# Performance work log

Measured on AMD Instinct MI355X. Metric: run time of the kernel, lower is better.

## Reference

```python
import jax, jax.numpy as jnp
import numpy as np
from jax import lax

B, T, C, H, N = 8, 2048, 1024, 16, 64  # dim=C=H*N


def setup_inputs() -> dict:
    key = jax.random.key(0)
    ks = jax.random.split(key, 12)
    s = 0.02
    return {
        "x": jax.random.normal(ks[0], (B, T, C), jnp.float32),
        "v_first": jnp.zeros((B, T, C), jnp.float32),  # unused for layer_id=0
        "ln1_w": jnp.ones((C,), jnp.float32),
        "ln1_b": jnp.zeros((C,), jnp.float32),
        "ln2_w": jnp.ones((C,), jnp.float32),
        "ln2_b": jnp.zeros((C,), jnp.float32),
        "w_r": jax.random.normal(ks[1], (C, C), jnp.float32) * s,
        "w_k": jax.random.normal(ks[2], (C, C), jnp.float32) * s,
        "w_v": jax.random.normal(ks[3], (C, C), jnp.float32) * s,
        "w_o": jax.random.normal(ks[4], (C, C), jnp.float32) * s,
        "w_g": jax.random.normal(ks[5], (H, C), jnp.float32) * s,
        "ck_w": jax.random.normal(ks[6], (4 * C, C), jnp.float32) * s,
        "cv_w": jax.random.normal(ks[7], (C, 4 * C), jnp.float32) * s,
    }


def _time_shift(x):
    # ZeroPad2d((0,0,1,-1)): zero at t=0, drop last timestep
    return jnp.pad(x, ((0, 0), (1, 0), (0, 0)))[:, :-1]


def _layernorm(x, w, b, eps=1e-5):
    mu = jnp.mean(x, axis=-1, keepdims=True)
    var = jnp.var(x, axis=-1, keepdims=True)
    return (x - mu) * lax.rsqrt(var + eps) * w + b


def _wkv(r, k, v):
    # wkv[0] = v[0]; wkv[t] = (wkv[t-1] + v[t]) / 2  (k is unused, faithful to source)
    vt = jnp.moveaxis(v, 1, 0)  # [T,B,H,N]

    def step(carry, v_t):
        s = 0.5 * (carry + v_t)
        return s, s

    # init carry = v[0] => first output = 0.5*(v0+v0) = v0, matching wkv[0]=v[0]
    _, out = lax.scan(step, vt[0], vt)
    return r * jnp.moveaxis(out, 0, 1)


def reference(x, v_first, ln1_w, ln1_b, ln2_w, ln2_b,
              w_r, w_k, w_v, w_o, w_g, ck_w, cv_w):
    # ---- TimeMixBiDirectional on ln1(x) ----
    h = _layernorm(x, ln1_w, ln1_b)
    xx = _time_shift(h) - h
    hs = h + xx  # == time-shifted h
    r = (hs @ w_r.T).reshape(B, T, H, N)
    k = (hs @ w_k.T).reshape(B, T, H, N)
    v_flat = hs @ w_v.T
    v_first_out = v_flat  # layer_id == 0
    v = v_flat.reshape(B, T, H, N)

    x_fwd = _wkv(r, k, v)
    x_bwd = jnp.flip(
        _wkv(jnp.flip(r, 1), jnp.flip(k, 1), jnp.flip(v, 1)), 1)

    gate = jax.nn.sigmoid(xx @ w_g.T)[..., None]  # [B,T,H,1]
    x_comb = gate * x_fwd + (1.0 - gate) * x_bwd
    attn_out = x_comb.reshape(B, T, C) @ w_o.T

    x1 = x + attn_out

    # ---- ChannelMix on ln2(x1) ----
    h2 = _layernorm(x1, ln2_w, ln2_b)
    k2 = _time_shift(h2)  # h2 + (shift(h2) - h2)
    k2 = jnp.square(jax.nn.relu(k2 @ ck_w.T))
    ffn_out = k2 @ cv_w.T

    return (x1 + ffn_out, v_first_out)
```

## Files before the change

### kernel.cpp

```cpp
#include <hip/hip_runtime.h>

constexpr int B_ = 8, T_ = 2048, C_ = 1024, H_ = 16, N_ = 64;
constexpr int M_ = B_ * T_;
constexpr int FC_ = 4 * C_;

typedef __attribute__((ext_vector_type(8))) short bf16x8;
typedef __attribute__((ext_vector_type(4))) float f32x4;
typedef unsigned short ushort_t;
typedef unsigned int uint_t;

__device__ __forceinline__ float bfu2f(ushort_t u) {
    union { uint_t i; float f; } c; c.i = ((uint_t)u) << 16; return c.f;
}
__device__ __forceinline__ ushort_t f2bfu(float f) {
    union { float f; uint_t i; } c; c.f = f;
    uint_t i = c.i;
    uint_t r = i + 0x7FFFu + ((i >> 16) & 1u);
    return (ushort_t)(r >> 16);
}

__device__ __forceinline__ void gl_lds16(const void* g, void* l) {
    __builtin_amdgcn_global_load_lds(
        (const __attribute__((address_space(1))) void*)g,
        (__attribute__((address_space(3))) void*)l, 16, 0, 0);
}

__global__ __launch_bounds__(256) void f2bf3_kernel(const float* __restrict__ a,
                                                    const float* __restrict__ b,
                                                    const float* __restrict__ c,
                                                    ushort_t* __restrict__ oa,
                                                    ushort_t* __restrict__ ob,
                                                    ushort_t* __restrict__ oc) {
    const float* in = (blockIdx.y == 0) ? a : (blockIdx.y == 1) ? b : c;
    ushort_t* out   = (blockIdx.y == 0) ? oa : (blockIdx.y == 1) ? ob : oc;
    size_t i = ((size_t)blockIdx.x * 256 + threadIdx.x) * 4;
    float4 v = *(const float4*)(in + i);
    uint2 o;
    o.x = (uint_t)f2bfu(v.x) | ((uint_t)f2bfu(v.y) << 16);
    o.y = (uint_t)f2bfu(v.z) | ((uint_t)f2bfu(v.w) << 16);
    *(uint2*)(out + i) = o;
}

__global__ __launch_bounds__(256) void f2bf2_kernel(const float* __restrict__ a,
                                                    const float* __restrict__ b,
                                                    ushort_t* __restrict__ oa,
                                                    ushort_t* __restrict__ ob) {
    const float* in = (blockIdx.y == 0) ? a : b;
    ushort_t* out   = (blockIdx.y == 0) ? oa : ob;
    size_t i = ((size_t)blockIdx.x * 256 + threadIdx.x) * 4;
    float4 v = *(const float4*)(in + i);
    uint2 o;
    o.x = (uint_t)f2bfu(v.x) | ((uint_t)f2bfu(v.y) << 16);
    o.y = (uint_t)f2bfu(v.z) | ((uint_t)f2bfu(v.w) << 16);
    *(uint2*)(out + i) = o;
}

__global__ __launch_bounds__(256) void ln_kernel(const float* __restrict__ x,
                                                 const float* __restrict__ w,
                                                 const float* __restrict__ b,
                                                 ushort_t* __restrict__ out) {
    const int row = blockIdx.x;
    const int tid = threadIdx.x;
    const float* xr = x + (size_t)row * C_;
    float4 xv = ((const float4*)xr)[tid];
    float s  = xv.x + xv.y + xv.z + xv.w;
    float ss = xv.x*xv.x + xv.y*xv.y + xv.z*xv.z + xv.w*xv.w;
#pragma unroll
    for (int off = 32; off; off >>= 1) { s += __shfl_down(s, off); ss += __shfl_down(ss, off); }
    __shared__ float sb[8];
    const int wv = tid >> 6, ln = tid & 63;
    if (ln == 0) { sb[wv] = s; sb[4 + wv] = ss; }
    __syncthreads();
    s  = sb[0] + sb[1] + sb[2] + sb[3];
    ss = sb[4] + sb[5] + sb[6] + sb[7];
    const float mean = s * (1.f / C_);
    const float var  = ss * (1.f / C_) - mean * mean;
    const float rstd = rsqrtf(var + 1e-5f);
    float4 wv4 = ((const float4*)w)[tid];
    float4 bv4 = ((const float4*)b)[tid];
    uint2 o;
    o.x = (uint_t)f2bfu((xv.x - mean) * rstd * wv4.x + bv4.x)
        | ((uint_t)f2bfu((xv.y - mean) * rstd * wv4.y + bv4.y) << 16);
    o.y = (uint_t)f2bfu((xv.z - mean) * rstd * wv4.z + bv4.z)
        | ((uint_t)f2bfu((xv.w - mean) * rstd * wv4.w + bv4.w) << 16);
    ((uint2*)(out + (size_t)row * C_))[tid] = o;
}

__global__ __launch_bounds__(256) void gate_kernel(const ushort_t* __restrict__ h,
                                                   const float* __restrict__ wg,
                                                   float* __restrict__ gate) {
    __shared__ float xr[C_];
    const int row = blockIdx.x;
    const int tid = threadIdx.x;
    const int t = row & (T_ - 1);
    uint2 cu = *(const uint2*)(h + (size_t)row * C_ + tid * 4);
    uint2 pu = make_uint2(0u, 0u);
    if (t > 0) pu = *(const uint2*)(h + (size_t)(row - 1) * C_ + tid * 4);
    xr[tid * 4 + 0] = bfu2f((ushort_t)(pu.x & 0xffffu)) - bfu2f((ushort_t)(cu.x & 0xffffu));
    xr[tid * 4 + 1] = bfu2f((ushort_t)(pu.x >> 16))     - bfu2f((ushort_t)(cu.x >> 16));
    xr[tid * 4 + 2] = bfu2f((ushort_t)(pu.y & 0xffffu)) - bfu2f((ushort_t)(cu.y & 0xffffu));
    xr[tid * 4 + 3] = bfu2f((ushort_t)(pu.y >> 16))     - bfu2f((ushort_t)(cu.y >> 16));
    __syncthreads();
    const int wv = tid >> 6, ln = tid & 63;
#pragma unroll
    for (int hh = 0; hh < 4; ++hh) {
        const int h_ = wv * 4 + hh;
        const float* wrow = wg + (size_t)h_ * C_;
        float acc = 0.f;
#pragma unroll
        for (int i = 0; i < 16; ++i) { int c = i * 64 + ln; acc += xr[c] * wrow[c]; }
#pragma unroll
        for (int off = 32; off; off >>= 1) acc += __shfl_down(acc, off);
        if (ln == 0) gate[(size_t)row * H_ + h_] = 1.f / (1.f + __expf(-acc));
    }
}

__global__ __launch_bounds__(128) void wkv_combine_kernel(const float* __restrict__ v,
                                                          const ushort_t* __restrict__ r,
                                                          const float* __restrict__ gate,
                                                          ushort_t* __restrict__ xc) {
    __shared__ float fbuf[128 * 64];
    __shared__ float bbuf[128 * 64];
    const int blk = blockIdx.x;
    const int chunk = blk & 15;
    const int bh = blk >> 4;
    const int h = bh & 15;
    const int b = bh >> 4;
    const int t0 = chunk * 128, t1 = t0 + 128;
    const int tid = threadIdx.x;
    const int n = tid & 63;
    const float* vb = v + (size_t)b * T_ * C_ + h * 64 + n;
    if (tid < 64) {
        int ts = t0 - 32; if (ts < 0) ts = 0;
        float carry = vb[(size_t)ts * C_];
        if (ts >= t0) fbuf[(ts - t0) * 64 + n] = carry;
        for (int t = ts + 1; t < t1; ++t) {
            carry = 0.5f * (carry + vb[(size_t)t * C_]);
            if (t >= t0) fbuf[(t - t0) * 64 + n] = carry;
        }
    } else {
        int ts = t1 - 1 + 32; if (ts > T_ - 1) ts = T_ - 1;
        float carry = vb[(size_t)ts * C_];
        if (ts < t1) bbuf[(ts - t0) * 64 + n] = carry;
        for (int t = ts - 1; t >= t0; --t) {
            carry = 0.5f * (carry + vb[(size_t)t * C_]);
            if (t < t1) bbuf[(t - t0) * 64 + n] = carry;
        }
    }
    __syncthreads();
#pragma unroll 4
    for (int i = 0; i < 64; ++i) {
        int idx = i * 128 + tid;
        int tl = idx >> 6, nn = idx & 63;
        size_t mrow = (size_t)b * T_ + (t0 + tl);
        float g = gate[mrow * H_ + h];
        float rr = bfu2f(r[mrow * C_ + h * 64 + nn]);
        float val = rr * (g * fbuf[tl * 64 + nn] + (1.f - g) * bbuf[tl * 64 + nn]);
        xc[mrow * C_ + h * 64 + nn] = f2bfu(val);
    }
}

#define LDS_FENCE() asm volatile("" ::: "memory")
#define PHASE_BAR() do { __builtin_amdgcn_sched_barrier(0); LDS_FENCE(); \
                         __builtin_amdgcn_s_barrier(); \
                         LDS_FENCE(); __builtin_amdgcn_sched_barrier(0); } while (0)
#define SETP(x) __builtin_amdgcn_s_setprio(x)

template <int EPI, bool SHIFT>
__global__ __launch_bounds__(512, 2) void gemm256(const ushort_t* __restrict__ A,
                                                  const ushort_t* __restrict__ Bm,
                                                  const float* __restrict__ extra,
                                                  float* __restrict__ outF,
                                                  ushort_t* __restrict__ outB,
                                                  const ushort_t* __restrict__ zpage,
                                                  int N, int K) {
    __shared__ ushort_t As[2][256 * 64];
    __shared__ ushort_t Bs[2][256 * 64];
    const int NT = K >> 6;
    const int tid = threadIdx.x;
    const int lane = tid & 63, wv = tid >> 6;
    const int wm = wv >> 2, wn = wv & 3;
    const size_t m0 = (size_t)(blockIdx.x & 63) * 256;
    const size_t n0 = (size_t)(blockIdx.x >> 6) * 256;

    const int l8 = lane >> 3;
    const int swcol = ((lane & 7) ^ l8) * 8;
    const ushort_t* pA[2][2];
    const ushort_t* pB[2][2];
#pragma unroll
    for (int hf = 0; hf < 2; ++hf)
#pragma unroll
        for (int i8 = 0; i8 < 2; ++i8) {
            const size_t tr = (size_t)(hf * 128 + wv * 16 + i8 * 8 + l8);
            const size_t mrow = m0 + tr, nrow = n0 + tr;
            if (SHIFT)
                pA[hf][i8] = ((mrow & (size_t)(T_ - 1)) == 0)
                                 ? (zpage + swcol)
                                 : (A + (mrow - 1) * (size_t)K + swcol);
            else
                pA[hf][i8] = A + mrow * (size_t)K + swcol;
            pB[hf][i8] = Bm + nrow * (size_t)K + swcol;
        }

    const int rl = lane & 15;
    const int swz = (lane & 7) << 4;
    const int cq = (lane >> 4) << 4;
    const int offk0 = cq ^ swz;
    const int offk1 = (64 | cq) ^ swz;
    const int aRow = (wm * 128 + rl) * 128;
    const int bRow = (wn * 64 + rl) * 128;

    bf16x8 a[8], b[8];
    f32x4 acc[8][4];
#pragma unroll
    for (int i = 0; i < 8; ++i)
#pragma unroll
        for (int j = 0; j < 4; ++j) acc[i][j] = (f32x4){0.f, 0.f, 0.f, 0.f};

#define STAGE_A(BUF, HF, KOF) do { \
    gl_lds16(pA[HF][0] + (KOF), &As[BUF][((HF) * 128 + wv * 16 + 0) * 64]); \
    gl_lds16(pA[HF][1] + (KOF), &As[BUF][((HF) * 128 + wv * 16 + 8) * 64]); } while (0)
#define STAGE_B(BUF, HF, KOF) do { \
    gl_lds16(pB[HF][0] + (KOF), &Bs[BUF][((HF) * 128 + wv * 16 + 0) * 64]); \
    gl_lds16(pB[HF][1] + (KOF), &Bs[BUF][((HF) * 128 + wv * 16 + 8) * 64]); } while (0)
#define LOAD_A(BUF, QM) do { \
    const char* _ab = (const char*)As[BUF] + aRow + (QM) * 64 * 128; \
    _Pragma("unroll") \
    for (int mi = 0; mi < 4; ++mi) { \
        a[mi * 2 + 0] = *(const bf16x8*)(_ab + mi * 16 * 128 + offk0); \
        a[mi * 2 + 1] = *(const bf16x8*)(_ab + mi * 16 * 128 + offk1); } } while (0)
#define LOAD_B(BUF, QN) do { \
    const char* _bb = (const char*)Bs[BUF] + bRow + (QN) * 32 * 128; \
    _Pragma("unroll") \
    for (int ni = 0; ni < 2; ++ni) { \
        b[((QN) * 2 + ni) * 2 + 0] = *(const bf16x8*)(_bb + ni * 16 * 128 + offk0); \
        b[((QN) * 2 + ni) * 2 + 1] = *(const bf16x8*)(_bb + ni * 16 * 128 + offk1); } } while (0)
#define MFMA_Q(QM, QN) do { \
    _Pragma("unroll") \
    for (int mi = 0; mi < 4; ++mi) \
    _Pragma("unroll") \
    for (int ni = 0; ni < 2; ++ni) { \
        acc[(QM)*4+mi][(QN)*2+ni] = __builtin_amdgcn_mfma_f32_16x16x32_bf16( \
            a[mi*2+0], b[((QN)*2+ni)*2+0], acc[(QM)*4+mi][(QN)*2+ni], 0, 0, 0); \
        acc[(QM)*4+mi][(QN)*2+ni] = __builtin_amdgcn_mfma_f32_16x16x32_bf16( \
            a[mi*2+1], b[((QN)*2+ni)*2+1], acc[(QM)*4+mi][(QN)*2+ni], 0, 0, 0); } } while (0)

#define KTILE(CB, OB, KT) do { \
    const int _kA = ((KT) + 1 < NT) ? ((KT) + 1) * 64 : 0; \
    const int _kB = ((KT) + 2 < NT) ? ((KT) + 2) * 64 : 0; \
    LOAD_A(CB, 0); LOAD_B(CB, 0); STAGE_A(OB, 0, _kA); \
    PHASE_BAR(); SETP(1); MFMA_Q(0, 0); SETP(0); PHASE_BAR(); \
    LOAD_B(CB, 1); STAGE_A(OB, 1, _kA); \
    PHASE_BAR(); SETP(1); MFMA_Q(0, 1); SETP(0); PHASE_BAR(); \
    LOAD_A(CB, 1); STAGE_B(CB, 0, _kB); \
    PHASE_BAR(); SETP(1); MFMA_Q(1, 1); SETP(0); PHASE_BAR(); \
    STAGE_B(CB, 1, _kB); \
    PHASE_BAR(); SETP(1); MFMA_Q(1, 0); SETP(0); \
    asm volatile("s_waitcnt vmcnt(4)" ::: "memory"); \
    PHASE_BAR(); } while (0)

    STAGE_B(0, 0, 0); STAGE_B(0, 1, 0);
    STAGE_A(0, 0, 0); STAGE_A(0, 1, 0);
    const int _k1 = 64;
    STAGE_B(1, 0, _k1); STAGE_B(1, 1, _k1);
    asm volatile("s_waitcnt vmcnt(4)" ::: "memory");
    PHASE_BAR();

    for (int kt = 0; kt < NT; kt += 2) {
        KTILE(0, 1, kt);
        KTILE(1, 0, kt + 1);
    }

#undef KTILE
#undef MFMA_Q
#undef LOAD_B
#undef LOAD_A
#undef STAGE_B
#undef STAGE_A

    const int crow = (lane >> 4) * 4;
    const int ccol = lane & 15;
#pragma unroll
    for (int mi = 0; mi < 8; ++mi) {
#pragma unroll
        for (int ni = 0; ni < 4; ++ni) {
#pragma unroll
            for (int rr = 0; rr < 4; ++rr) {
                size_t row = m0 + wm * 128 + mi * 16 + crow + rr;
                size_t col = n0 + wn * 64 + ni * 16 + ccol;
                size_t oix = row * (size_t)N + col;
                float v = acc[mi][ni][rr];
                if (EPI == 0)      outB[oix] = f2bfu(v);
                else if (EPI == 1) outF[oix] = v;
                else if (EPI == 2) outF[oix] = extra[oix] + v;
                else { float t = v > 0.f ? v : 0.f; outB[oix] = f2bfu(t * t); }
            }
        }
    }
}

extern "C" void kernel_launch(void* const* d_in, const int* in_sizes, int n_in,
                              void* d_out, int out_size, void* d_ws, size_t ws_size,
                              hipStream_t stream) {
    const float* x    = (const float*)d_in[0];
    const float* ln1w = (const float*)d_in[2];
    const float* ln1b = (const float*)d_in[3];
    const float* ln2w = (const float*)d_in[4];
    const float* ln2b = (const float*)d_in[5];
    const float* w_r  = (const float*)d_in[6];
    const float* w_v  = (const float*)d_in[8];
    const float* w_o  = (const float*)d_in[9];
    const float* w_g  = (const float*)d_in[10];
    const float* ck_w = (const float*)d_in[11];
    const float* cv_w = (const float*)d_in[12];

    float* out0 = (float*)d_out;
    float* vout = out0 + (size_t)M_ * C_;

    char* ws = (char*)d_ws;
    const size_t MB = 1024ull * 1024ull;
    ushort_t* wr_bf = (ushort_t*)(ws + 0 * MB);
    ushort_t* wv_bf = (ushort_t*)(ws + 2 * MB);
    ushort_t* wo_bf = (ushort_t*)(ws + 4 * MB);
    ushort_t* ck_bf = (ushort_t*)(ws + 6 * MB);
    ushort_t* cv_bf = (ushort_t*)(ws + 14 * MB);
    float*    gate  = (float*)(ws + 22 * MB);
    ushort_t* zpage = (ushort_t*)(ws + 23 * MB);
    ushort_t* bufA  = (ushort_t*)(ws + 24 * MB);
    ushort_t* bufC  = (ushort_t*)(ws + 56 * MB);
    ushort_t* r_bf  = (ushort_t*)(ws + 88 * MB);
    float*    x1    = (float*)(ws + 120 * MB);
    ushort_t* k2p   = (ushort_t*)(ws + 184 * MB);

    f2bf3_kernel<<<dim3(C_ * C_ / 1024, 3), 256, 0, stream>>>(w_r, w_v, w_o, wr_bf, wv_bf, wo_bf);
    f2bf2_kernel<<<dim3(FC_ * C_ / 1024, 2), 256, 0, stream>>>(ck_w, cv_w, ck_bf, cv_bf);
    hipMemsetAsync(zpage, 0, 16384, stream);

    ln_kernel<<<M_, 256, 0, stream>>>(x, ln1w, ln1b, bufA);

    gate_kernel<<<M_, 256, 0, stream>>>(bufA, w_g, gate);

    gemm256<0, true><<<(M_ / 256) * (C_ / 256), 512, 0, stream>>>(bufA, wr_bf, nullptr, nullptr, r_bf, zpage, C_, C_);
    gemm256<1, true><<<(M_ / 256) * (C_ / 256), 512, 0, stream>>>(bufA, wv_bf, nullptr, vout, nullptr, zpage, C_, C_);

    wkv_combine_kernel<<<B_ * H_ * (T_ / 128), 128, 0, stream>>>(vout, r_bf, gate, bufC);

    gemm256<2, false><<<(M_ / 256) * (C_ / 256), 512, 0, stream>>>(bufC, wo_bf, x, x1, nullptr, zpage, C_, C_);

    ln_kernel<<<M_, 256, 0, stream>>>(x1, ln2w, ln2b, bufA);

    gemm256<3, true><<<(M_ / 256) * (FC_ / 256), 512, 0, stream>>>(bufA, ck_bf, nullptr, nullptr, k2p, zpage, FC_, C_);
    gemm256<2, false><<<(M_ / 256) * (C_ / 256), 512, 0, stream>>>(k2p, cv_bf, x1, out0, nullptr, zpage, C_, FC_);
}
```

Measured before the change: 881.1 us.

## Restructure GEMM k-loop to prefetch LDS fragments across phases with fewer barriers

Reworks the 256x256 bf16 GEMM main loop so that LDS fragment loads for the next quadrant, and for the next k-tile, are issued while the current MFMA quadrant runs. B fragments go into two register sets, and the quadrant order changes so A fragments are reused. Barriers drop from eight to four per k-tile, and scheduler barriers are applied more selectively, letting the compiler interleave ds_reads with MFMAs. This adds register pressure under the 512-thread, 2-block launch bounds, and the vmcnt and barrier placement is delicate for correctness.

Result: faster. 844.6 us (-4.1%).

```diff
diff --git a/kernel.cpp b/kernel.cpp
--- a/kernel.cpp
+++ b/kernel.cpp
@@ -160,11 +160,12 @@
     }
 }
 
-#define LDS_FENCE() asm volatile("" ::: "memory")
-#define PHASE_BAR() do { __builtin_amdgcn_sched_barrier(0); LDS_FENCE(); \
-                         __builtin_amdgcn_s_barrier(); \
-                         LDS_FENCE(); __builtin_amdgcn_sched_barrier(0); } while (0)
+#define BAR() do { asm volatile("" ::: "memory"); \
+                   __builtin_amdgcn_s_barrier(); \
+                   asm volatile("" ::: "memory"); } while (0)
 #define SETP(x) __builtin_amdgcn_s_setprio(x)
+#define SCHEDB() __builtin_amdgcn_sched_barrier(0)
+#define VMCNT(n) asm volatile("s_waitcnt vmcnt(" #n ")" ::: "memory")
 
 template <int EPI, bool SHIFT>
 __global__ __launch_bounds__(512, 2) void gemm256(const ushort_t* __restrict__ A,
@@ -210,7 +211,7 @@
     const int aRow = (wm * 128 + rl) * 128;
     const int bRow = (wn * 64 + rl) * 128;
 
-    bf16x8 a[8], b[8];
+    bf16x8 a[8], b0[4], b1[4];
     f32x4 acc[8][4];
 #pragma unroll
     for (int i = 0; i < 8; ++i)
@@ -223,48 +224,61 @@
 #define STAGE_B(BUF, HF, KOF) do { \
     gl_lds16(pB[HF][0] + (KOF), &Bs[BUF][((HF) * 128 + wv * 16 + 0) * 64]); \
     gl_lds16(pB[HF][1] + (KOF), &Bs[BUF][((HF) * 128 + wv * 16 + 8) * 64]); } while (0)
-#define LOAD_A(BUF, QM) do { \
+#define LOAD_A(ARR, BUF, QM) do { \
     const char* _ab = (const char*)As[BUF] + aRow + (QM) * 64 * 128; \
     _Pragma("unroll") \
     for (int mi = 0; mi < 4; ++mi) { \
-        a[mi * 2 + 0] = *(const bf16x8*)(_ab + mi * 16 * 128 + offk0); \
-        a[mi * 2 + 1] = *(const bf16x8*)(_ab + mi * 16 * 128 + offk1); } } while (0)
-#define LOAD_B(BUF, QN) do { \
+        ARR[mi * 2 + 0] = *(const bf16x8*)(_ab + mi * 16 * 128 + offk0); \
+        ARR[mi * 2 + 1] = *(const bf16x8*)(_ab + mi * 16 * 128 + offk1); } } while (0)
+#define LOAD_B(ARR, BUF, QN) do { \
     const char* _bb = (const char*)Bs[BUF] + bRow + (QN) * 32 * 128; \
     _Pragma("unroll") \
     for (int ni = 0; ni < 2; ++ni) { \
-        b[((QN) * 2 + ni) * 2 + 0] = *(const bf16x8*)(_bb + ni * 16 * 128 + offk0); \
-        b[((QN) * 2 + ni) * 2 + 1] = *(const bf16x8*)(_bb + ni * 16 * 128 + offk1); } } while (0)
-#define MFMA_Q(QM, QN) do { \
+        ARR[ni * 2 + 0] = *(const bf16x8*)(_bb + ni * 16 * 128 + offk0); \
+        ARR[ni * 2 + 1] = *(const bf16x8*)(_bb + ni * 16 * 128 + offk1); } } while (0)
+#define MFMA_Q(AARR, BARR, QM, QN) do { \
     _Pragma("unroll") \
     for (int mi = 0; mi < 4; ++mi) \
     _Pragma("unroll") \
     for (int ni = 0; ni < 2; ++ni) { \
         acc[(QM)*4+mi][(QN)*2+ni] = __builtin_amdgcn_mfma_f32_16x16x32_bf16( \
-            a[mi*2+0], b[((QN)*2+ni)*2+0], acc[(QM)*4+mi][(QN)*2+ni], 0, 0, 0); \
+            AARR[mi*2+0], BARR[ni*2+0], acc[(QM)*4+mi][(QN)*2+ni], 0, 0, 0); \
         acc[(QM)*4+mi][(QN)*2+ni] = __builtin_amdgcn_mfma_f32_16x16x32_bf16( \
-            a[mi*2+1], b[((QN)*2+ni)*2+1], acc[(QM)*4+mi][(QN)*2+ni], 0, 0, 0); } } while (0)
+            AARR[mi*2+1], BARR[ni*2+1], acc[(QM)*4+mi][(QN)*2+ni], 0, 0, 0); } } while (0)
 
 #define KTILE(CB, OB, KT) do { \
     const int _kA = ((KT) + 1 < NT) ? ((KT) + 1) * 64 : 0; \
     const int _kB = ((KT) + 2 < NT) ? ((KT) + 2) * 64 : 0; \
-    LOAD_A(CB, 0); LOAD_B(CB, 0); STAGE_A(OB, 0, _kA); \
-    PHASE_BAR(); SETP(1); MFMA_Q(0, 0); SETP(0); PHASE_BAR(); \
-    LOAD_B(CB, 1); STAGE_A(OB, 1, _kA); \
-    PHASE_BAR(); SETP(1); MFMA_Q(0, 1); SETP(0); PHASE_BAR(); \
-    LOAD_A(CB, 1); STAGE_B(CB, 0, _kB); \
-    PHASE_BAR(); SETP(1); MFMA_Q(1, 1); SETP(0); PHASE_BAR(); \
+    BAR(); \
+    LOAD_B(b1, CB, 1); \
+    STAGE_A(OB, 0, _kA); \
+    SETP(1); MFMA_Q(a, b0, 0, 0); SETP(0); \
+    BAR(); \
+    STAGE_A(OB, 1, _kA); \
+    SETP(1); MFMA_Q(a, b1, 0, 1); SETP(0); \
+    SCHEDB(); \
+    LOAD_A(a, CB, 1); \
+    VMCNT(4); \
+    BAR(); \
+    STAGE_B(CB, 0, _kB); \
+    SETP(1); MFMA_Q(a, b0, 1, 0); SETP(0); \
+    VMCNT(2); \
+    BAR(); \
+    LOAD_B(b0, OB, 0); \
     STAGE_B(CB, 1, _kB); \
-    PHASE_BAR(); SETP(1); MFMA_Q(1, 0); SETP(0); \
-    asm volatile("s_waitcnt vmcnt(4)" ::: "memory"); \
-    PHASE_BAR(); } while (0)
-
+    SETP(1); MFMA_Q(a, b1, 1, 1); SETP(0); \
+    SCHEDB(); \
+    LOAD_A(a, OB, 0); \
+  } while (0)
+
+    STAGE_A(0, 0, 0); STAGE_A(0, 1, 0);
     STAGE_B(0, 0, 0); STAGE_B(0, 1, 0);
-    STAGE_A(0, 0, 0); STAGE_A(0, 1, 0);
-    const int _k1 = 64;
+    const int _k1 = (NT > 1) ? 64 : 0;
     STAGE_B(1, 0, _k1); STAGE_B(1, 1, _k1);
-    asm volatile("s_waitcnt vmcnt(4)" ::: "memory");
-    PHASE_BAR();
+    VMCNT(4);
+    BAR();
+    LOAD_A(a, 0, 0);
+    LOAD_B(b0, 0, 0);
 
     for (int kt = 0; kt < NT; kt += 2) {
         KTILE(0, 1, kt);
```
